# Kernel tuning notes

Measured on AMD Instinct MI355X. Metric: run time of the kernel, lower is better.

The kernel has to match this reference:

```python
import jax, jax.numpy as jnp
import numpy as np

T = 0.15
ALPHA = 1.0
EPS = 1e-8  # torch.cosine_similarity eps


def setup_inputs() -> dict:
    key = jax.random.key(0)
    k1, k2 = jax.random.split(key)
    x = jax.random.normal(k1, (4096, 1024), dtype=jnp.float32)
    y = jax.random.normal(k2, (4096, 1024), dtype=jnp.float32)
    return {"x": x, "y": y}


def reference(x, y):
    N = x.shape[0]
    nx = jnp.linalg.norm(x, axis=1)  # [N]
    ny = jnp.linalg.norm(y, axis=1)  # [N]

    # positive pairs: cos(x_i, y_i)/T -> exp
    pos = jnp.exp(jnp.sum(x * y, axis=1) / jnp.maximum(nx * ny, EPS) / T)  # [N]

    # pairwise exp-cosine matrices via GEMM (replaces N^2 python loop)
    Sxx = jnp.exp((x @ x.T) / jnp.maximum(nx[:, None] * nx[None, :], EPS) / T)
    Sxy = jnp.exp((x @ y.T) / jnp.maximum(nx[:, None] * ny[None, :], EPS) / T)

    mask = 1.0 - jnp.eye(N, dtype=x.dtype)  # i != j only
    row_sums = jnp.sum((Sxx + Sxy) * mask, axis=1)  # [N]
    # FAITHFUL to source bug: accumulator `sum` never reset across i -> cumulative
    neg = jnp.cumsum(row_sums)  # [N]

    nce_loss = -jnp.sum(jnp.log(pos / neg))

    # JS divergence with batchmean KL (torch KLDivLoss(log_mean, target))
    a = jax.nn.softmax(x, axis=1)
    b = jax.nn.softmax(y, axis=1)
    log_mean = jnp.log((a + b) * 0.5)
    kl_a = jnp.sum(a * (jnp.log(a) - log_mean)) / N
    kl_b = jnp.sum(b * (jnp.log(b) - log_mean)) / N
    js_loss = (kl_a + kl_b) * 0.5

    loss = nce_loss + ALPHA * js_loss
    return loss.reshape(1)
```

## Files before the change

### kernel.cpp

```cpp
#include <hip/hip_runtime.h>
#include <stdint.h>

#define N_ROWS 4096
#define D_DIM  1024
#define ROWB   1024
#define T_TEMP 0.15f

#define AS1 __attribute__((address_space(1)))
#define AS3 __attribute__((address_space(3)))

typedef float f32x4  __attribute__((ext_vector_type(4)));
typedef int   i32x4v __attribute__((ext_vector_type(4)));

__device__ __forceinline__ float wsum(float v) {
#pragma unroll
  for (int m = 32; m >= 1; m >>= 1) v += __shfl_xor(v, m, 64);
  return v;
}
__device__ __forceinline__ float wmax(float v) {
#pragma unroll
  for (int m = 32; m >= 1; m >>= 1) v = fmaxf(v, __shfl_xor(v, m, 64));
  return v;
}

__global__ __launch_bounds__(256) void prep_kernel(
    const float* __restrict__ x, const float* __restrict__ y,
    unsigned char* __restrict__ Bb, float* __restrict__ inv_n,
    float* __restrict__ logpos, float* __restrict__ js,
    float* __restrict__ rowsum) {
  if (threadIdx.x < 4) rowsum[blockIdx.x * 4 + threadIdx.x] = 0.0f;

  const int wid = threadIdx.x >> 6, lane = threadIdx.x & 63;
  const int row = blockIdx.x * 4 + wid;
  const float4* xp = (const float4*)(x + (size_t)row * D_DIM) + lane * 4;
  const float4* yp = (const float4*)(y + (size_t)row * D_DIM) + lane * 4;

  float xv[16], yv[16];
#pragma unroll
  for (int i = 0; i < 4; ++i) {
    float4 a = xp[i], b = yp[i];
    xv[i*4+0]=a.x; xv[i*4+1]=a.y; xv[i*4+2]=a.z; xv[i*4+3]=a.w;
    yv[i*4+0]=b.x; yv[i*4+1]=b.y; yv[i*4+2]=b.z; yv[i*4+3]=b.w;
  }

  float sx2=0.f, sy2=0.f, sxy=0.f, mx=-1e30f, my=-1e30f;
#pragma unroll
  for (int k = 0; k < 16; ++k) {
    sx2 = fmaf(xv[k], xv[k], sx2);
    sy2 = fmaf(yv[k], yv[k], sy2);
    sxy = fmaf(xv[k], yv[k], sxy);
    mx = fmaxf(mx, xv[k]); my = fmaxf(my, yv[k]);
  }
  sx2 = wsum(sx2); sy2 = wsum(sy2); sxy = wsum(sxy);
  mx = wmax(mx);  my = wmax(my);

  float ex[16], ey[16], sex=0.f, sey=0.f;
#pragma unroll
  for (int k = 0; k < 16; ++k) {
    ex[k] = __expf(xv[k] - mx); ey[k] = __expf(yv[k] - my);
    sex += ex[k]; sey += ey[k];
  }
  sex = wsum(sex); sey = wsum(sey);
  const float lsex = __logf(sex), lsey = __logf(sey);
  const float rsex = 1.f / sex,  rsey = 1.f / sey;

  float term = 0.f;
#pragma unroll
  for (int k = 0; k < 16; ++k) {
    float a = ex[k] * rsex, b = ey[k] * rsey;
    float lm = __logf(0.5f * (a + b));
    term += a * ((xv[k] - mx - lsex) - lm) + b * ((yv[k] - my - lsey) - lm);
  }
  term = wsum(term);

  if (lane == 0) {
    const float nx = sqrtf(sx2), ny = sqrtf(sy2);
    inv_n[row] = 1.f / nx;
    inv_n[N_ROWS + row] = 1.f / ny;
    logpos[row] = sxy / fmaxf(nx * ny, 1e-8f) / T_TEMP;
    js[row] = term;
  }

  int p[4], q[4];
#pragma unroll
  for (int w = 0; w < 4; ++w) {
    int v = 0;
    v = __builtin_amdgcn_cvt_pk_fp8_f32(xv[w*4+0], xv[w*4+1], v, false);
    v = __builtin_amdgcn_cvt_pk_fp8_f32(xv[w*4+2], xv[w*4+3], v, true);
    p[w] = v;
    int u = 0;
    u = __builtin_amdgcn_cvt_pk_fp8_f32(yv[w*4+0], yv[w*4+1], u, false);
    u = __builtin_amdgcn_cvt_pk_fp8_f32(yv[w*4+2], yv[w*4+3], u, true);
    q[w] = u;
  }
  const int ktp = lane >> 2;
  const int lq  = lane & 3;
  const int kkb = lq >> 1;
  const int h0  = (lq & 1) * 2;
  {
    char* ob = (char*)Bb + (size_t)row * ROWB + ktp * 64 + kkb * 8 + h0 * 16;
    *(int2*)(ob)      = make_int2(p[0], p[1]);
    *(int2*)(ob + 16) = make_int2(p[2], p[3]);
    char* oy = (char*)Bb + (size_t)(N_ROWS + row) * ROWB + ktp * 64 + kkb * 8 + h0 * 16;
    *(int2*)(oy)      = make_int2(q[0], q[1]);
    *(int2*)(oy + 16) = make_int2(q[2], q[3]);
  }
}

#define GLL(src, dst) __builtin_amdgcn_global_load_lds((const AS1 void*)(src), (AS3 void*)(dst), 16, 0, 0)

__global__ __launch_bounds__(256, 3) void gemm_fused(
    const unsigned char* __restrict__ Bb, const float* __restrict__ inv_n,
    float* __restrict__ rowsum) {
  __shared__ __align__(16) char As[2 * 8192];
  __shared__ __align__(16) char Bs[2 * 8192];
  const int tid = threadIdx.x;
  const int wid = tid >> 6, lane = tid & 63;
  const int lo = lane & 15, hi = lane >> 4;

  int bi, bj;
  bool sym = false;
  {
    const int idx = blockIdx.x;
    if (idx < 1024) {
      bi = idx >> 5; bj = 32 + (idx & 31);
    } else {
      const int t = idx - 1024;
      int b = (int)((65.0 - sqrt((double)(4225 - 8 * t))) * 0.5);
      while ((b + 1) * (65 - (b + 1)) / 2 <= t) ++b;
      while (b * (65 - b) / 2 > t) --b;
      bi = b;
      bj = b + (t - b * (65 - b) / 2);
      sym = (bi != bj);
    }
  }
  const int grow0 = bi * 128;
  const int gcol0 = bj * 128;
  const int wrow = (wid >> 1) * 64, wcol = (wid & 1) * 64;

  f32x4 acc[4][4] = {};

  const int sr = tid >> 2;
  const int sh = (tid & 3) ^ ((tid >> 3) & 3);
  const char* gA = (const char*)Bb + (size_t)(grow0 + sr) * ROWB + sh * 16;
  const char* gB = (const char*)Bb + (size_t)(gcol0 + sr) * ROWB + sh * 16;
  char* dA = As + tid * 16;
  char* dB = Bs + tid * 16;

  const int xr = (lo >> 1) & 3;
  const int rslot = (hi ^ xr) * 16;

  union U { i32x4v v; long l[2]; };

  for (int kt = 0; kt < 8; ++kt) {
    __syncthreads();
#pragma unroll
    for (int q = 0; q < 4; ++q) {
      const size_t goff = (size_t)((q & 1) * 64) * ROWB + (q >> 1) * 64 + kt * 128;
      GLL(gA + goff, dA + q * 4096);
      GLL(gB + goff, dB + q * 4096);
    }
    __syncthreads();

#pragma unroll
    for (int gi = 0; gi < 2; ++gi) {
      U a[4];
#pragma unroll
      for (int m = 0; m < 4; ++m)
        a[m].v = *(const i32x4v*)(As + gi * 8192 + (wrow + m * 16 + lo) * 64 + rslot);
#pragma unroll
      for (int n = 0; n < 4; ++n) {
        U bv;
        bv.v = *(const i32x4v*)(Bs + gi * 8192 + (wcol + n * 16 + lo) * 64 + rslot);
#pragma unroll
        for (int m = 0; m < 4; ++m) {
          acc[m][n] = __builtin_amdgcn_mfma_f32_16x16x32_fp8_fp8(
              a[m].l[0], bv.l[0], acc[m][n], 0, 0, 0);
          acc[m][n] = __builtin_amdgcn_mfma_f32_16x16x32_fp8_fp8(
              a[m].l[1], bv.l[1], acc[m][n], 0, 0, 0);
        }
      }
    }
  }

  const float C = 1.4426950408889634f / T_TEMP;
  float invc[4], invr[4][4];
#pragma unroll
  for (int n = 0; n < 4; ++n)
    invc[n] = inv_n[gcol0 + wcol + n * 16 + lo] * C;
#pragma unroll
  for (int m = 0; m < 4; ++m)
#pragma unroll
    for (int r = 0; r < 4; ++r)
      invr[m][r] = inv_n[grow0 + wrow + m * 16 + hi * 4 + r];

  float rp[4][4] = {};
  float cp[4] = {};
#pragma unroll
  for (int m = 0; m < 4; ++m)
#pragma unroll
    for (int n = 0; n < 4; ++n)
#pragma unroll
      for (int r = 0; r < 4; ++r) {
        const int i = grow0 + wrow + m * 16 + hi * 4 + r;
        const int j = gcol0 + wcol + n * 16 + lo;
        float e2 = exp2f(acc[m][n][r] * invr[m][r] * invc[n]);
        if (j == i || j == i + N_ROWS) e2 = 0.0f;
        rp[m][r] += e2;
        cp[n] += e2;
      }

#pragma unroll
  for (int m = 0; m < 4; ++m)
#pragma unroll
    for (int r = 0; r < 4; ++r) {
      float v = rp[m][r];
      v += __shfl_xor(v, 1, 16);
      v += __shfl_xor(v, 2, 16);
      v += __shfl_xor(v, 4, 16);
      v += __shfl_xor(v, 8, 16);
      if (lo == 0)
        atomicAdd(&rowsum[grow0 + wrow + m * 16 + hi * 4 + r], v);
    }

  if (sym) {
#pragma unroll
    for (int n = 0; n < 4; ++n) {
      float v = cp[n];
      v += __shfl_xor(v, 16, 64);
      v += __shfl_xor(v, 32, 64);
      if (hi == 0)
        atomicAdd(&rowsum[gcol0 + wcol + n * 16 + lo], v);
    }
  }
}

__global__ __launch_bounds__(256) void final_kernel(
    const float* __restrict__ rowsum, const float* __restrict__ logpos,
    const float* __restrict__ js, float* __restrict__ out) {
  __shared__ float scan[256];
  __shared__ double ds[4];
  __shared__ float fs[4];
  const int tid = threadIdx.x;
  float loc[16];
  float run = 0.f, jl = 0.f;
#pragma unroll
  for (int k = 0; k < 16; ++k) {
    loc[k] = rowsum[tid * 16 + k];
    run += loc[k];
    jl += js[tid * 16 + k];
  }
  scan[tid] = run;
  __syncthreads();
  for (int d = 1; d < 256; d <<= 1) {
    float add = (tid >= d) ? scan[tid - d] : 0.0f;
    __syncthreads();
    scan[tid] += add;
    __syncthreads();
  }
  float c = scan[tid] - run;
  double acc = 0.0;
#pragma unroll
  for (int k = 0; k < 16; ++k) {
    c += loc[k];
    acc += (double)(logf(c) - logpos[tid * 16 + k]);
  }
#pragma unroll
  for (int m = 32; m >= 1; m >>= 1) {
    acc += __shfl_xor(acc, m, 64);
    jl  += __shfl_xor(jl, m, 64);
  }
  if ((tid & 63) == 0) { ds[tid >> 6] = acc; fs[tid >> 6] = jl; }
  __syncthreads();
  if (tid == 0) {
    const double nce = ds[0] + ds[1] + ds[2] + ds[3];
    const double jst = (double)(fs[0] + fs[1] + fs[2] + fs[3]);
    out[0] = (float)(nce + jst / (2.0 * N_ROWS));
  }
}

extern "C" void kernel_launch(void* const* d_in, const int* in_sizes, int n_in,
                              void* d_out, int out_size, void* d_ws, size_t ws_size,
                              hipStream_t stream) {
  const float* x = (const float*)d_in[0];
  const float* y = (const float*)d_in[1];
  float* out = (float*)d_out;

  char* ws = (char*)d_ws;
  unsigned char* Bb = (unsigned char*)ws;
  float* inv_n  = (float*)(ws + (size_t)8 * 1024 * 1024);
  float* logpos = inv_n + 8192;
  float* rowsum = logpos + 4096;
  float* js     = rowsum + 4096;

  prep_kernel<<<N_ROWS / 4, 256, 0, stream>>>(x, y, Bb, inv_n, logpos, js, rowsum);
  gemm_fused<<<1552, 256, 0, stream>>>(Bb, inv_n, rowsum);
  final_kernel<<<1, 256, 0, stream>>>(rowsum, logpos, js, out);
}
```

Measured before the change: 68.52 us.

## Double-buffer LDS staging in FP8 Gram GEMM to overlap loads with MFMA

The K loop of the symmetric Gram GEMM now works on 64-byte K chunks instead of 128-byte ones. The LDS is split into two buffers and the next chunk is prefetched by direct global-to-LDS loads while the MFMAs run on the current buffer. This replaces the two-barrier load-then-compute sequence with one barrier per iteration, so memory latency can hide behind compute. The trade-off is twice as many iterations with less work each, and it relies on the existing LDS size holding both buffers.

After: 72.69 us. 6.1% more time.

```diff
diff --git a/kernel.cpp b/kernel.cpp
--- a/kernel.cpp
+++ b/kernel.cpp
@@ -144,43 +144,42 @@
   const int sh = (tid & 3) ^ ((tid >> 3) & 3);
   const char* gA = (const char*)Bb + (size_t)(grow0 + sr) * ROWB + sh * 16;
   const char* gB = (const char*)Bb + (size_t)(gcol0 + sr) * ROWB + sh * 16;
-  char* dA = As + tid * 16;
-  char* dB = Bs + tid * 16;
+
+#define STG(kt_, b_) do { \
+    GLL(gA + (size_t)(kt_) * 64,                      As + (b_) * 8192 + tid * 16); \
+    GLL(gA + 64 * (size_t)ROWB + (size_t)(kt_) * 64,  As + (b_) * 8192 + 4096 + tid * 16); \
+    GLL(gB + (size_t)(kt_) * 64,                      Bs + (b_) * 8192 + tid * 16); \
+    GLL(gB + 64 * (size_t)ROWB + (size_t)(kt_) * 64,  Bs + (b_) * 8192 + 4096 + tid * 16); \
+  } while (0)
 
   const int xr = (lo >> 1) & 3;
   const int rslot = (hi ^ xr) * 16;
 
   union U { i32x4v v; long l[2]; };
 
-  for (int kt = 0; kt < 8; ++kt) {
+  STG(0, 0);
+  __syncthreads();
+
+  for (int kt = 0; kt < 16; ++kt) {
+    const int b = kt & 1;
+    U a[4], bv[4];
+#pragma unroll
+    for (int m = 0; m < 4; ++m)
+      a[m].v = *(const i32x4v*)(As + b * 8192 + (wrow + m * 16 + lo) * 64 + rslot);
+#pragma unroll
+    for (int n = 0; n < 4; ++n)
+      bv[n].v = *(const i32x4v*)(Bs + b * 8192 + (wcol + n * 16 + lo) * 64 + rslot);
+    if (kt < 15) STG(kt + 1, b ^ 1);
+#pragma unroll
+    for (int n = 0; n < 4; ++n)
+#pragma unroll
+      for (int m = 0; m < 4; ++m) {
+        acc[m][n] = __builtin_amdgcn_mfma_f32_16x16x32_fp8_fp8(
+            a[m].l[0], bv[n].l[0], acc[m][n], 0, 0, 0);
+        acc[m][n] = __builtin_amdgcn_mfma_f32_16x16x32_fp8_fp8(
+            a[m].l[1], bv[n].l[1], acc[m][n], 0, 0, 0);
+      }
     __syncthreads();
-#pragma unroll
-    for (int q = 0; q < 4; ++q) {
-      const size_t goff = (size_t)((q & 1) * 64) * ROWB + (q >> 1) * 64 + kt * 128;
-      GLL(gA + goff, dA + q * 4096);
-      GLL(gB + goff, dB + q * 4096);
-    }
-    __syncthreads();
-
-#pragma unroll
-    for (int gi = 0; gi < 2; ++gi) {
-      U a[4];
-#pragma unroll
-      for (int m = 0; m < 4; ++m)
-        a[m].v = *(const i32x4v*)(As + gi * 8192 + (wrow + m * 16 + lo) * 64 + rslot);
-#pragma unroll
-      for (int n = 0; n < 4; ++n) {
-        U bv;
-        bv.v = *(const i32x4v*)(Bs + gi * 8192 + (wcol + n * 16 + lo) * 64 + rslot);
-#pragma unroll
-        for (int m = 0; m < 4; ++m) {
-          acc[m][n] = __builtin_amdgcn_mfma_f32_16x16x32_fp8_fp8(
-              a[m].l[0], bv.l[0], acc[m][n], 0, 0, 0);
-          acc[m][n] = __builtin_amdgcn_mfma_f32_16x16x32_fp8_fp8(
-              a[m].l[1], bv.l[1], acc[m][n], 0, 0, 0);
-        }
-      }
-    }
   }
 
   const float C = 1.4426950408889634f / T_TEMP;
@@ -233,6 +232,7 @@
         atomicAdd(&rowsum[gcol0 + wcol + n * 16 + lo], v);
     }
   }
+#undef STG
 }
 
 __global__ __launch_bounds__(256) void final_kernel(
```
